# Optimization experiments

Hardware: AMD Instinct MI355X
Metric: run time of the kernel (lower is better)

The kernel has to match this reference:

```python
import jax, jax.numpy as jnp
import numpy as np

MAX_DISP = 192


def setup_inputs() -> dict:
    key = jax.random.key(0)
    k1, k2 = jax.random.split(key)
    B, C, H, W = 4, 32, 64, 128
    left_feats = jax.random.normal(k1, (B, C, H, W), dtype=jnp.float32)
    right_feats = jax.random.normal(k2, (B, C, H, W), dtype=jnp.float32)
    return {"left_feats": left_feats, "right_feats": right_feats}


def build_cost(left_feats, right_feats, max_disp=MAX_DISP):
    B, C, H, W = left_feats.shape
    D = max_disp // 4
    d = jnp.arange(D)[:, None]          # [D,1]
    w = jnp.arange(W)[None, :]          # [1,W]
    mask = (w >= d).astype(left_feats.dtype)  # [D,W]
    # left half: cost[:, :C, d, :, w] = left[:, :, :, w] for w >= d, else 0
    left_part = left_feats[:, :, None, :, :] * mask[None, None, :, None, :]  # [B,C,D,H,W]
    # right half: cost[:, C:, d, :, w] = right[:, :, :, w-d] for w >= d, else 0
    idx = jnp.clip(w - d, 0, W - 1)     # [D,W]
    right_gather = right_feats[:, :, :, idx]            # [B,C,H,D,W]
    right_part = jnp.transpose(right_gather, (0, 1, 3, 2, 4)) * mask[None, None, :, None, :]
    return jnp.concatenate([left_part, right_part], axis=1)  # [B,2C,D,H,W]


def reference(left_feats, right_feats):
    return build_cost(left_feats, right_feats)
```

## Files before the change

kernel.cpp:

```cpp
#include <hip/hip_runtime.h>


#define BB 4
#define CC 32
#define HH 64
#define WW 128
#define DD 48

typedef float vfloat4 __attribute__((ext_vector_type(4)));

__global__ __launch_bounds__(256) void cost_kernel(
    const float* __restrict__ left,
    const float* __restrict__ right,
    float* __restrict__ out)
{
    const int p  = blockIdx.x * 256 + threadIdx.x;
    const int bc = blockIdx.z;
    const int b  = bc >> 6;
    const int c2 = bc & 63;
    const int h  = p >> 5;
    const int k0 = p & 31;
    const int w0 = k0 * 4;

    const bool is_right = (c2 >= CC);
    const int  c        = is_right ? (c2 - CC) : c2;
    const float* __restrict__ src = is_right ? right : left;
    const vfloat4* __restrict__ row4 =
        reinterpret_cast<const vfloat4*>(src + ((((size_t)b * CC + c) * HH + h) * WW));

    const int stride4 = HH * WW / 4;
    vfloat4* __restrict__ out4 = reinterpret_cast<vfloat4*>(out)
                               + (size_t)bc * DD * stride4 + p;

    if (!is_right) {
        const vfloat4 lv = row4[k0];
        #pragma unroll
        for (int d = 0; d < DD; ++d) {
            vfloat4 o;
            o.x = (w0 + 0 >= d) ? lv.x : 0.0f;
            o.y = (w0 + 1 >= d) ? lv.y : 0.0f;
            o.z = (w0 + 2 >= d) ? lv.z : 0.0f;
            o.w = (w0 + 3 >= d) ? lv.w : 0.0f;
            __builtin_nontemporal_store(o, out4 + (size_t)d * stride4);
        }
    } else {
        vfloat4 b4 = row4[k0];
        int k = k0;
        #pragma unroll
        for (int g = 0; g < DD / 4; ++g) {
            vfloat4 a4 = (vfloat4)(0.0f);
            if (k >= 1) a4 = row4[k - 1];

            const vfloat4 o0 = b4;
            vfloat4 o1; o1.x = a4.w; o1.y = b4.x; o1.z = b4.y; o1.w = b4.z;
            vfloat4 o2; o2.x = a4.z; o2.y = a4.w; o2.z = b4.x; o2.w = b4.y;
            vfloat4 o3; o3.x = a4.y; o3.y = a4.z; o3.z = a4.w; o3.w = b4.x;

            __builtin_nontemporal_store(o0, out4 + (size_t)(4 * g + 0) * stride4);
            __builtin_nontemporal_store(o1, out4 + (size_t)(4 * g + 1) * stride4);
            __builtin_nontemporal_store(o2, out4 + (size_t)(4 * g + 2) * stride4);
            __builtin_nontemporal_store(o3, out4 + (size_t)(4 * g + 3) * stride4);

            b4 = a4;
            --k;
        }
    }
}

extern "C" void kernel_launch(void* const* d_in, const int* in_sizes, int n_in,
                              void* d_out, int out_size, void* d_ws, size_t ws_size,
                              hipStream_t stream)
{
    const float* left  = (const float*)d_in[0];
    const float* right = (const float*)d_in[1];
    float* out = (float*)d_out;

    dim3 grid(HH * WW / 4 / 256, 1, BB * 2 * CC);
    cost_kernel<<<grid, dim3(256), 0, stream>>>(left, right, out);
}
```

Baseline: 391.6 us.

## Switch to grid-stride flat output indexing with persistent 1024-block grid

Replaces the per-(b,c,pixel) thread that loops over all 48 disparities with a flat grid-stride loop. Each thread now writes one float4 output element per iteration across a fixed 1024-block grid, so consecutive threads write contiguous memory. Stores change from nontemporal to regular, and every output element rereads its input row vectors instead of reusing them in registers. The goal is fully sequential write streams for this store-bound kernel, at the cost of redundant input loads and per-element index arithmetic.

Measured after the change: 447.0 us. 14.2% more time.

```diff
diff --git a/kernel.cpp b/kernel.cpp
--- a/kernel.cpp
+++ b/kernel.cpp
@@ -7,6 +7,13 @@
 #define WW 128
 #define DD 48
 
+#define SLAB4 (HH * WW / 4)
+#define BC4   (DD * SLAB4)
+#define N4    (BB * 2 * CC * BC4)
+#define NBLK  1024
+#define NTHR  (NBLK * 256)
+#define ITERS (N4 / NTHR)
+
 typedef float vfloat4 __attribute__((ext_vector_type(4)));
 
 __global__ __launch_bounds__(256) void cost_kernel(
@@ -14,56 +21,50 @@
     const float* __restrict__ right,
     float* __restrict__ out)
 {
-    const int p  = blockIdx.x * 256 + threadIdx.x;
-    const int bc = blockIdx.z;
-    const int b  = bc >> 6;
-    const int c2 = bc & 63;
-    const int h  = p >> 5;
-    const int k0 = p & 31;
-    const int w0 = k0 * 4;
+    int idx = blockIdx.x * 256 + threadIdx.x;
+    vfloat4* __restrict__ out4 = reinterpret_cast<vfloat4*>(out);
 
-    const bool is_right = (c2 >= CC);
-    const int  c        = is_right ? (c2 - CC) : c2;
-    const float* __restrict__ src = is_right ? right : left;
-    const vfloat4* __restrict__ row4 =
-        reinterpret_cast<const vfloat4*>(src + ((((size_t)b * CC + c) * HH + h) * WW));
+    #pragma unroll 4
+    for (int it = 0; it < ITERS; ++it, idx += NTHR) {
+        const int bc = idx / BC4;
+        const int r1 = idx - bc * BC4;
+        const int d  = r1 >> 11;
+        const int p  = idx & (SLAB4 - 1);
+        const int h  = p >> 5;
+        const int k0 = p & 31;
+        const int w0 = k0 * 4;
 
-    const int stride4 = HH * WW / 4;
-    vfloat4* __restrict__ out4 = reinterpret_cast<vfloat4*>(out)
-                               + (size_t)bc * DD * stride4 + p;
+        const int  b        = bc >> 6;
+        const bool is_right = (bc & 32) != 0;
+        const int  c        = bc & 31;
+        const float* __restrict__ src = is_right ? right : left;
+        const vfloat4* __restrict__ row4 = reinterpret_cast<const vfloat4*>(
+            src + (((size_t)(b * CC + c) * HH + h) * WW));
 
-    if (!is_right) {
-        const vfloat4 lv = row4[k0];
-        #pragma unroll
-        for (int d = 0; d < DD; ++d) {
-            vfloat4 o;
+        vfloat4 o;
+        if (!is_right) {
+            const vfloat4 lv = row4[k0];
             o.x = (w0 + 0 >= d) ? lv.x : 0.0f;
             o.y = (w0 + 1 >= d) ? lv.y : 0.0f;
             o.z = (w0 + 2 >= d) ? lv.z : 0.0f;
             o.w = (w0 + 3 >= d) ? lv.w : 0.0f;
-            __builtin_nontemporal_store(o, out4 + (size_t)d * stride4);
+        } else {
+            const int q = d >> 2;
+            const int s = d & 3;
+            const int j = k0 - q;
+            vfloat4 Bv = (vfloat4)(0.0f);
+            vfloat4 Av = (vfloat4)(0.0f);
+            if (j >= 0) Bv = row4[j];
+            if (j >= 1) Av = row4[j - 1];
+            switch (s) {
+                case 0:  o = Bv; break;
+                case 1:  o.x = Av.w; o.y = Bv.x; o.z = Bv.y; o.w = Bv.z; break;
+                case 2:  o.x = Av.z; o.y = Av.w; o.z = Bv.x; o.w = Bv.y; break;
+                default: o.x = Av.y; o.y = Av.z; o.z = Av.w; o.w = Bv.x; break;
+            }
         }
-    } else {
-        vfloat4 b4 = row4[k0];
-        int k = k0;
-        #pragma unroll
-        for (int g = 0; g < DD / 4; ++g) {
-            vfloat4 a4 = (vfloat4)(0.0f);
-            if (k >= 1) a4 = row4[k - 1];
 
-            const vfloat4 o0 = b4;
-            vfloat4 o1; o1.x = a4.w; o1.y = b4.x; o1.z = b4.y; o1.w = b4.z;
-            vfloat4 o2; o2.x = a4.z; o2.y = a4.w; o2.z = b4.x; o2.w = b4.y;
-            vfloat4 o3; o3.x = a4.y; o3.y = a4.z; o3.z = a4.w; o3.w = b4.x;
-
-            __builtin_nontemporal_store(o0, out4 + (size_t)(4 * g + 0) * stride4);
-            __builtin_nontemporal_store(o1, out4 + (size_t)(4 * g + 1) * stride4);
-            __builtin_nontemporal_store(o2, out4 + (size_t)(4 * g + 2) * stride4);
-            __builtin_nontemporal_store(o3, out4 + (size_t)(4 * g + 3) * stride4);
-
-            b4 = a4;
-            --k;
-        }
+        out4[idx] = o;
     }
 }
 
@@ -75,6 +76,5 @@
     const float* right = (const float*)d_in[1];
     float* out = (float*)d_out;
 
-    dim3 grid(HH * WW / 4 / 256, 1, BB * 2 * CC);
-    cost_kernel<<<grid, dim3(256), 0, stream>>>(left, right, out);
+    cost_kernel<<<dim3(NBLK), dim3(256), 0, stream>>>(left, right, out);
 }
```
